# Performance work log

Hardware: AMD Instinct MI355X
Metric: run time of the kernel (lower is better)

## Reference

```python
import jax, jax.numpy as jnp
import numpy as np

B, T, D = 4, 2048, 1024


def ste_sign(x):
    # forward: sign(x); backward: identity (straight-through)
    return jax.lax.stop_gradient(jnp.sign(x) - x) + x


def setup_inputs() -> dict:
    key = jax.random.key(0)
    kx, kq, kk, kv = jax.random.split(key, 4)
    return {
        "x": jax.random.normal(kx, (B, T, D), dtype=jnp.float32),
        "bv_q": jax.random.normal(kq, (D,), dtype=jnp.float32) * 0.02,
        "bv_k": jax.random.normal(kk, (D,), dtype=jnp.float32) * 0.02,
        "bv_v": jax.random.normal(kv, (D,), dtype=jnp.float32) * 0.02,
    }


def reference(x, bv_q, bv_k, bv_v):
    d = x.shape[-1]
    scale = d ** (-0.5)
    bq = ste_sign(bv_q)
    bk = ste_sign(bv_k)
    bv = ste_sign(bv_v)
    Q = ste_sign(x * bq)          # [B,T,D], values in {-1,0,1}
    K = ste_sign(x * bk)
    V = x * bv                    # [B,T,D]
    scores = jnp.einsum('btd,bsd->bts', Q, K) * scale  # [B,T,T]
    t = x.shape[1]
    causal = jnp.tril(jnp.ones((t, t), dtype=bool))    # [T,T]
    scores = jnp.where(causal, scores, -jnp.inf)
    attn = jax.nn.sigmoid(scores * 4.0)
    attn = jnp.where(causal, attn, 0.0)
    return jnp.einsum('bts,bsd->btd', attn, V)
```

## Files before the change

### kernel.cpp

```cpp
#include <hip/hip_runtime.h>
#include <hip/hip_bf16.h>
#include <stdint.h>
#include <math.h>

#define B_SZ 4
#define T_SZ 2048
#define D_SZ 1024

constexpr int NTH = 512;

typedef short bf16x8 __attribute__((ext_vector_type(8)));
typedef float f32x4 __attribute__((ext_vector_type(4)));
typedef int i32x4 __attribute__((ext_vector_type(4)));
typedef unsigned short ushort8 __attribute__((ext_vector_type(8)));

__device__ __forceinline__ uint32_t sbf(uint32_t xu, uint32_t su) {
  return 0x3F80u | (((xu ^ su) >> 16) & 0x8000u);
}

__device__ __forceinline__ ushort f2bf(float f) {
  uint32_t u = __float_as_uint(f);
  return (ushort)((u + 0x7FFFu + ((u >> 16) & 1u)) >> 16);
}

__device__ __forceinline__ void glds16(const void* g, void* l) {
  __builtin_amdgcn_global_load_lds(
      (const __attribute__((address_space(1))) void*)g,
      (__attribute__((address_space(3))) void*)l, 16, 0, 0);
}

__global__ __launch_bounds__(256) void prep_kernel(
    const float* __restrict__ x, const float* __restrict__ bvq,
    const float* __restrict__ bvk, const float* __restrict__ bvv,
    char* __restrict__ Qb, char* __restrict__ Kb, ushort* __restrict__ Vt) {
  __shared__ ushort vt[64][72];
  const int bid = blockIdx.x;
  const int dt = bid & 15;
  const int tt = (bid >> 4) & 31;
  const int b = bid >> 9;
  const int t0 = tt * 64, d0 = dt * 64;
  const int tid = threadIdx.x;

#pragma unroll
  for (int p = 0; p < 4; ++p) {
    const int row = p * 16 + (tid >> 4);
    const int c4 = tid & 15;
    const size_t idx = ((size_t)(b * T_SZ + t0 + row)) * D_SZ + d0 + c4 * 4;
    float4 v = *(const float4*)(x + idx);
    float4 q = *(const float4*)(bvq + d0 + c4 * 4);
    float4 k = *(const float4*)(bvk + d0 + c4 * 4);
    float4 s = *(const float4*)(bvv + d0 + c4 * 4);
    uint32_t xu[4] = {__float_as_uint(v.x), __float_as_uint(v.y),
                      __float_as_uint(v.z), __float_as_uint(v.w)};
    uint32_t qu[4] = {__float_as_uint(q.x), __float_as_uint(q.y),
                      __float_as_uint(q.z), __float_as_uint(q.w)};
    uint32_t ku[4] = {__float_as_uint(k.x), __float_as_uint(k.y),
                      __float_as_uint(k.z), __float_as_uint(k.w)};
    uint32_t su[4] = {__float_as_uint(s.x), __float_as_uint(s.y),
                      __float_as_uint(s.z), __float_as_uint(s.w)};
    uint32_t qw = 0, kw = 0;
#pragma unroll
    for (int j = 0; j < 4; ++j) {
      uint32_t qb = ((xu[j] ^ qu[j]) & 0x80000000u) ? 0xFFu : 0x01u;
      uint32_t kb = ((xu[j] ^ ku[j]) & 0x80000000u) ? 0xFFu : 0x01u;
      qw |= qb << (8 * j);
      kw |= kb << (8 * j);
      vt[row][c4 * 4 + j] = f2bf(__uint_as_float(xu[j] ^ (su[j] & 0x80000000u)));
    }
    *(uint32_t*)(Qb + idx) = qw;
    *(uint32_t*)(Kb + idx) = kw;
  }
  __syncthreads();
#pragma unroll
  for (int p = 0; p < 2; ++p) {
    const int dr = p * 32 + (tid >> 3);
    const int tc = tid & 7;
    ushort8 o;
#pragma unroll
    for (int j = 0; j < 8; ++j) o[j] = vt[tc * 8 + j][dr];
    *(ushort8*)(Vt + ((size_t)(b * D_SZ + d0 + dr)) * T_SZ + t0 + tc * 8) = o;
  }
}

__global__ __launch_bounds__(NTH) void score_kernel(
    const char* __restrict__ Qb, const char* __restrict__ Kb,
    ushort* __restrict__ P) {
  __shared__ __align__(16) unsigned char Qs[2][128 * 128];
  __shared__ __align__(16) unsigned char Ks[2][128 * 128];

  const int bid = blockIdx.x;
  const int xcd = bid & 7;
  const int b = xcd >> 1;
  const int j = ((bid >> 3) << 1) + (xcd & 1);
  int qt = (int)((sqrtf(8.f * (float)j + 1.f) - 1.f) * 0.5f);
  while ((qt + 1) * (qt + 2) / 2 <= j) ++qt;
  while (qt * (qt + 1) / 2 > j) --qt;
  const int st = j - qt * (qt + 1) / 2;

  const int tid = threadIdx.x;
  const int lane = tid & 63, w = tid >> 6;
  const int wr = w >> 1, wc = w & 1;
  const int l15 = lane & 15, l4 = lane >> 4;

  const size_t qrow0 = ((size_t)(b * T_SZ + qt * 128)) * D_SZ;
  const size_t krow0 = ((size_t)(b * T_SZ + st * 128)) * D_SZ;

  i32x4 sacc[2][4];
#pragma unroll
  for (int mf = 0; mf < 2; ++mf)
#pragma unroll
    for (int nf = 0; nf < 4; ++nf) sacc[mf][nf] = (i32x4){0, 0, 0, 0};

  auto STAGE = [&](int buf, int ks) {
#pragma unroll
    for (int i = 0; i < 4; ++i) {
      const int isK = i >> 1;
      const int fi = tid + (i & 1) * 512;
      const int row = fi >> 3, c = fi & 7;
      const int cs = c ^ (row & 7);
      const char* src = (isK ? Kb + krow0 : Qb + qrow0) +
                        (size_t)row * D_SZ + ks * 128 + cs * 16;
      unsigned char* dst = (isK ? Ks[buf] : Qs[buf]) + fi * 16;
      glds16(src, dst);
    }
  };

  STAGE(0, 0);
  for (int ks = 0; ks < 8; ++ks) {
    asm volatile("s_waitcnt vmcnt(0)" ::: "memory");
    __builtin_amdgcn_s_barrier();
    if (ks + 1 < 8) STAGE((ks + 1) & 1, ks + 1);
    const int buf = ks & 1;
#pragma unroll
    for (int kc = 0; kc < 2; ++kc) {
      i32x4 af[2], bfr[4];
#pragma unroll
      for (int mf = 0; mf < 2; ++mf) {
        const int row = wr * 32 + mf * 16 + l15;
        const int ch = (kc * 4 + l4) ^ (row & 7);
        af[mf] = *(const i32x4*)(Qs[buf] + row * 128 + ch * 16);
      }
#pragma unroll
      for (int nf = 0; nf < 4; ++nf) {
        const int row = wc * 64 + nf * 16 + l15;
        const int ch = (kc * 4 + l4) ^ (row & 7);
        bfr[nf] = *(const i32x4*)(Ks[buf] + row * 128 + ch * 16);
      }
#pragma unroll
      for (int mf = 0; mf < 2; ++mf)
#pragma unroll
        for (int nf = 0; nf < 4; ++nf)
          sacc[mf][nf] = __builtin_amdgcn_mfma_i32_16x16x64_i8(
              af[mf], bfr[nf], sacc[mf][nf], 0, 0, 0);
    }
    asm volatile("s_waitcnt lgkmcnt(0)" ::: "memory");
  }

#pragma unroll
  for (int mf = 0; mf < 2; ++mf)
#pragma unroll
    for (int nf = 0; nf < 4; ++nf)
#pragma unroll
      for (int r = 0; r < 4; ++r) {
        const int qg = qt * 128 + wr * 32 + mf * 16 + l4 * 4 + r;
        const int sg = st * 128 + wc * 64 + nf * 16 + l15;
        float p = 1.f / (1.f + __expf(-0.125f * (float)sacc[mf][nf][r]));
        if (sg > qg) p = 0.f;
        P[((size_t)(b * T_SZ + qg)) * T_SZ + sg] = f2bf(p);
      }
}

__global__ __launch_bounds__(NTH, 4) void pv_kernel(
    const ushort* __restrict__ P, const ushort* __restrict__ Vt,
    float* __restrict__ out) {
  __shared__ __align__(16) unsigned char Pl[2][64 * 128];
  __shared__ __align__(16) unsigned char Vl[2][256 * 128];
  const int bid = blockIdx.x;
  const int xcd = bid & 7;
  const int t_ = bid >> 3;
  const int g = xcd + 8 * (t_ & 1);
  const int b = g >> 2;
  const int ds = g & 3;
  const int qt = 31 - (t_ >> 1);

  const int tid = threadIdx.x;
  const int lane = tid & 63, w = tid >> 6;
  const int wr = w >> 2, dg = w & 3;
  const int l15 = lane & 15, l4 = lane >> 4;

  const char* Pb = (const char*)P;
  const char* Vb = (const char*)Vt;
  const size_t vrow0 = ((size_t)(b * D_SZ + ds * 256)) * (T_SZ * 2);
  const size_t prow0 = ((size_t)(b * T_SZ + qt * 64)) * (T_SZ * 2);
  const int nst = qt + 1;

  auto STAGE = [&](int buf, int stt) {
    {
      const int row = tid >> 3, c = tid & 7;
      const int cs = c ^ (row & 7);
      glds16(Pb + prow0 + (size_t)row * (T_SZ * 2) + stt * 128 + cs * 16,
             Pl[buf] + tid * 16);
    }
#pragma unroll
    for (int i = 0; i < 4; ++i) {
      const int f = tid + i * 512;
      const int row = f >> 3, c = f & 7;
      const int cs = c ^ (row & 7);
      glds16(Vb + vrow0 + (size_t)row * (T_SZ * 2) + stt * 128 + cs * 16,
             Vl[buf] + f * 16);
    }
  };

  f32x4 acc[2][4];
#pragma unroll
  for (int mf = 0; mf < 2; ++mf)
#pragma unroll
    for (int nf = 0; nf < 4; ++nf) acc[mf][nf] = (f32x4){0.f, 0.f, 0.f, 0.f};

  STAGE(0, 0);

  for (int t = 0; t < nst; ++t) {
    asm volatile("s_waitcnt vmcnt(0)" ::: "memory");
    __builtin_amdgcn_s_barrier();
    if (t + 1 < nst) STAGE((t + 1) & 1, t + 1);
    const int buf = t & 1;
#pragma unroll
    for (int kk = 0; kk < 2; ++kk) {
      bf16x8 pa[2], vb[4];
#pragma unroll
      for (int mf = 0; mf < 2; ++mf) {
        const int row = wr * 32 + mf * 16 + l15;
        const int ch = (kk * 4 + l4) ^ (row & 7);
        pa[mf] = *(const bf16x8*)(Pl[buf] + row * 128 + ch * 16);
      }
#pragma unroll
      for (int nf = 0; nf < 4; ++nf) {
        const int row = dg * 64 + nf * 16 + l15;
        const int ch = (kk * 4 + l4) ^ (row & 7);
        vb[nf] = *(const bf16x8*)(Vl[buf] + row * 128 + ch * 16);
      }
#pragma unroll
      for (int mf = 0; mf < 2; ++mf)
#pragma unroll
        for (int nf = 0; nf < 4; ++nf)
          acc[mf][nf] = __builtin_amdgcn_mfma_f32_16x16x32_bf16(
              pa[mf], vb[nf], acc[mf][nf], 0, 0, 0);
    }
    asm volatile("s_waitcnt lgkmcnt(0)" ::: "memory");
  }

  float* ob = out + ((size_t)(b * T_SZ + qt * 64 + wr * 32)) * D_SZ +
              ds * 256 + dg * 64;
#pragma unroll
  for (int mf = 0; mf < 2; ++mf)
#pragma unroll
    for (int nf = 0; nf < 4; ++nf)
#pragma unroll
      for (int r = 0; r < 4; ++r)
        ob[(size_t)(mf * 16 + l4 * 4 + r) * D_SZ + nf * 16 + l15] =
            acc[mf][nf][r];
}

__global__ __launch_bounds__(NTH, 4) void attn_main(
    const char* __restrict__ Qb, const char* __restrict__ Kb,
    const ushort* __restrict__ Vt, float* __restrict__ out) {
  __shared__ __align__(16) unsigned char Qs[32][1040];
  __shared__ __align__(16) ushort Ps[32][72];
  const int tid = threadIdx.x;
  const int lane = tid & 63;
  const int w = tid >> 6;
  const int rg = w >> 2, cg = w & 3;
  const int l15 = lane & 15, l4 = lane >> 4;
  const int bid = blockIdx.x;
  const int half = bid & 1;
  const int ti = (bid >> 1) & 63;
  const int b = bid >> 7;
  const int t0 = ti * 32;
  {
    const int row = tid >> 4;
    const int c = (tid & 15) * 64;
    const uint4* src = (const uint4*)(Qb + ((size_t)(b * T_SZ + t0 + row)) * D_SZ + c);
    uint4 a0 = src[0], a1 = src[1], a2 = src[2], a3 = src[3];
    *(uint4*)&Qs[row][c] = a0;
    *(uint4*)&Qs[row][c + 16] = a1;
    *(uint4*)&Qs[row][c + 32] = a2;
    *(uint4*)&Qs[row][c + 48] = a3;
  }
  __syncthreads();
  const int nt = (t0 + 32 + 63) / 64;
  const int s_beg = half ? (nt + 1) / 2 : 0;
  const int s_end = half ? nt : (nt + 1) / 2;
  f32x4 acc[16];
#pragma unroll
  for (int f = 0; f < 16; ++f) acc[f] = (f32x4){0.f, 0.f, 0.f, 0.f};
  const unsigned char* qrow = &Qs[rg * 16 + l15][l4 * 16];
  for (int st = s_beg; st < s_end; ++st) {
    const int s0 = st * 64;
    i32x4 sacc = (i32x4){0, 0, 0, 0};
    const char* kbase = Kb + ((size_t)(b * T_SZ + s0 + cg * 16 + l15)) * D_SZ + l4 * 16;
#pragma unroll
    for (int kc = 0; kc < 16; ++kc) {
      i32x4 a = *(const i32x4*)(qrow + kc * 64);
      i32x4 kf = *(const i32x4*)(kbase + kc * 64);
      sacc = __builtin_amdgcn_mfma_i32_16x16x64_i8(a, kf, sacc, 0, 0, 0);
    }
    __syncthreads();
    {
      const int scol = cg * 16 + l15;
      const int sg = s0 + scol;
#pragma unroll
      for (int r = 0; r < 4; ++r) {
        const int m = rg * 16 + l4 * 4 + r;
        float p = 0.f;
        if (sg <= t0 + m) p = 1.f / (1.f + __expf(-0.125f * (float)sacc[r]));
        Ps[m][scol] = f2bf(p);
      }
    }
    __syncthreads();
    const ushort* vtb = Vt + ((size_t)(b * D_SZ + cg * 256)) * T_SZ + s0;
#pragma unroll
    for (int kk = 0; kk < 2; ++kk) {
      bf16x8 pa = *(const bf16x8*)&Ps[rg * 16 + l15][kk * 32 + l4 * 8];
      const ushort* vks = vtb + kk * 32 + l4 * 8;
#pragma unroll
      for (int f = 0; f < 16; ++f) {
        bf16x8 vb = *(const bf16x8*)(vks + (size_t)(f * 16 + l15) * T_SZ);
        acc[f] = __builtin_amdgcn_mfma_f32_16x16x32_bf16(pa, vb, acc[f], 0, 0, 0);
      }
    }
  }
  float* orow = out + ((size_t)(b * T_SZ + t0)) * D_SZ;
#pragma unroll
  for (int f = 0; f < 16; ++f) {
    const int n = cg * 256 + f * 16 + l15;
#pragma unroll
    for (int r = 0; r < 4; ++r) {
      const int m = rg * 16 + l4 * 4 + r;
      atomicAdd(orow + (size_t)m * D_SZ + n, acc[f][r]);
    }
  }
}

__global__ __launch_bounds__(NTH) void hdc_attn_fallback(
    const float* __restrict__ x, const float* __restrict__ bvq,
    const float* __restrict__ bvk, const float* __restrict__ bvv,
    float* __restrict__ out) {
  __shared__ ushort Qs[32][1032];
  __shared__ ushort Ks[64][72];
  __shared__ ushort Ps[32][72];
  const int tid = threadIdx.x;
  const int lane = tid & 63;
  const int w = tid >> 6;
  const int rg = w >> 2, cg = w & 3;
  const int l15 = lane & 15, l4 = lane >> 4;
  const int b = blockIdx.x >> 6;
  const int ti = blockIdx.x & 63;
  const int t0 = ti * 32;
  {
    const float4* xr = (const float4*)(x + ((size_t)b * T_SZ + t0) * D_SZ);
    const float4* bq4 = (const float4*)bvq;
#pragma unroll
    for (int i = 0; i < 16; ++i) {
      int flat4 = tid + i * NTH;
      int row = flat4 >> 8, c4 = flat4 & 255;
      float4 v = xr[row * 256 + c4];
      float4 q = bq4[c4];
      uint32_t q0 = sbf(__float_as_uint(v.x), __float_as_uint(q.x));
      uint32_t q1 = sbf(__float_as_uint(v.y), __float_as_uint(q.y));
      uint32_t q2 = sbf(__float_as_uint(v.z), __float_as_uint(q.z));
      uint32_t q3 = sbf(__float_as_uint(v.w), __float_as_uint(q.w));
      *(uint2*)&Qs[row][c4 * 4] = make_uint2(q0 | (q1 << 16), q2 | (q3 << 16));
    }
  }
  uint32_t vsign[16];
#pragma unroll
  for (int f = 0; f < 16; ++f)
    vsign[f] = __float_as_uint(bvv[cg * 256 + f * 16 + l15]) & 0x80000000u;
  f32x4 acc[16];
#pragma unroll
  for (int f = 0; f < 16; ++f) acc[f] = (f32x4){0.f, 0.f, 0.f, 0.f};
  const int nt = (t0 + 32 + 63) / 64;
  for (int st = 0; st < nt; ++st) {
    const int s0 = st * 64;
    f32x4 sacc = (f32x4){0.f, 0.f, 0.f, 0.f};
    for (int dc = 0; dc < D_SZ / 64; ++dc) {
      __syncthreads();
      {
        const int s = tid >> 3;
        const int c8 = (tid & 7) * 8;
        const float* xk = x + ((size_t)b * T_SZ + s0 + s) * D_SZ + dc * 64 + c8;
        const float* bk = bvk + dc * 64 + c8;
        float4 v0 = *(const float4*)xk;
        float4 v1 = *(const float4*)(xk + 4);
        float4 k0 = *(const float4*)bk;
        float4 k1 = *(const float4*)(bk + 4);
        uint32_t w0 = sbf(__float_as_uint(v0.x), __float_as_uint(k0.x)) |
                      (sbf(__float_as_uint(v0.y), __float_as_uint(k0.y)) << 16);
        uint32_t w1 = sbf(__float_as_uint(v0.z), __float_as_uint(k0.z)) |
                      (sbf(__float_as_uint(v0.w), __float_as_uint(k0.w)) << 16);
        uint32_t w2 = sbf(__float_as_uint(v1.x), __float_as_uint(k1.x)) |
                      (sbf(__float_as_uint(v1.y), __float_as_uint(k1.y)) << 16);
        uint32_t w3 = sbf(__float_as_uint(v1.z), __float_as_uint(k1.z)) |
                      (sbf(__float_as_uint(v1.w), __float_as_uint(k1.w)) << 16);
        *(uint4*)&Ks[s][c8] = make_uint4(w0, w1, w2, w3);
      }
      __syncthreads();
#pragma unroll
      for (int h = 0; h < 2; ++h) {
        bf16x8 a = *(const bf16x8*)&Qs[rg * 16 + l15][dc * 64 + h * 32 + l4 * 8];
        bf16x8 kb = *(const bf16x8*)&Ks[cg * 16 + l15][h * 32 + l4 * 8];
        sacc = __builtin_amdgcn_mfma_f32_16x16x32_bf16(a, kb, sacc, 0, 0, 0);
      }
    }
    {
      const int scol = cg * 16 + l15;
      const int sg = s0 + scol;
#pragma unroll
      for (int r = 0; r < 4; ++r) {
        const int m = rg * 16 + l4 * 4 + r;
        float p = 0.f;
        if (sg <= t0 + m) p = 1.f / (1.f + __expf(-0.125f * sacc[r]));
        Ps[m][scol] = (ushort)(__float_as_uint(p) >> 16);
      }
    }
    __syncthreads();
    const float* xv = x + ((size_t)b * T_SZ + s0) * D_SZ;
#pragma unroll
    for (int kk = 0; kk < 2; ++kk) {
      bf16x8 pa = *(const bf16x8*)&Ps[rg * 16 + l15][kk * 32 + l4 * 8];
      const float* xvs = xv + (size_t)(kk * 32 + l4 * 8) * D_SZ;
#pragma unroll
      for (int f = 0; f < 16; ++f) {
        const int n = cg * 256 + f * 16 + l15;
        const float* xn = xvs + n;
        bf16x8 vb;
#pragma unroll
        for (int i = 0; i < 8; ++i) {
          uint32_t u = __float_as_uint(xn[(size_t)i * D_SZ]) ^ vsign[f];
          vb[i] = (short)(u >> 16);
        }
        acc[f] = __builtin_amdgcn_mfma_f32_16x16x32_bf16(pa, vb, acc[f], 0, 0, 0);
      }
    }
  }
  float* orow = out + ((size_t)b * T_SZ + t0) * D_SZ;
#pragma unroll
  for (int f = 0; f < 16; ++f) {
    const int n = cg * 256 + f * 16 + l15;
#pragma unroll
    for (int r = 0; r < 4; ++r) {
      const int m = rg * 16 + l4 * 4 + r;
      orow[(size_t)m * D_SZ + n] = acc[f][r];
    }
  }
}

extern "C" void kernel_launch(void* const* d_in, const int* in_sizes, int n_in,
                              void* d_out, int out_size, void* d_ws, size_t ws_size,
                              hipStream_t stream) {
  const float* x = (const float*)d_in[0];
  const float* bvq = (const float*)d_in[1];
  const float* bvk = (const float*)d_in[2];
  const float* bvv = (const float*)d_in[3];
  float* out = (float*)d_out;

  const size_t QB_SZ = (size_t)B_SZ * T_SZ * D_SZ;
  const size_t VT_SZ = QB_SZ * 2;
  const size_t P_SZ = (size_t)B_SZ * T_SZ * T_SZ * 2;
  const size_t NEED_MID = QB_SZ * 2 + VT_SZ;
  const size_t NEED_FULL = NEED_MID + P_SZ;

  if (ws_size >= NEED_MID) {
    char* Qb = (char*)d_ws;
    char* Kb = Qb + QB_SZ;
    ushort* Vt = (ushort*)(Kb + QB_SZ);
    hipLaunchKernelGGL(prep_kernel, dim3(B_SZ * 32 * 16), dim3(256), 0, stream,
                       x, bvq, bvk, bvv, Qb, Kb, Vt);
    if (ws_size >= NEED_FULL) {
      ushort* P = (ushort*)((char*)d_ws + NEED_MID);
      hipLaunchKernelGGL(score_kernel, dim3(544), dim3(NTH), 0, stream,
                         Qb, Kb, P);
      hipLaunchKernelGGL(pv_kernel, dim3(512), dim3(NTH), 0, stream,
                         P, Vt, out);
    } else {
      hipMemsetAsync(out, 0, (size_t)out_size * sizeof(float), stream);
      hipLaunchKernelGGL(attn_main, dim3(B_SZ * 64 * 2), dim3(NTH), 0, stream,
                         Qb, Kb, Vt, out);
    }
  } else {
    hipLaunchKernelGGL(hdc_attn_fallback, dim3(B_SZ * 64), dim3(NTH), 0, stream,
                       x, bvq, bvk, bvv, out);
  }
}
```

Before: 74.33 us.

## Store P and V in MFMA-fragment tiled layout and read directly in pv_kernel

prep_kernel and score_kernel now write V and P in a blocked 16x8 fragment layout that matches the MFMA operand shape. This lets pv_kernel load operands straight from global memory with contiguous 16-byte reads instead of staging through LDS. pv_kernel now uses 256 threads with 128-wide d slices, and each block handles a pair of q-tiles (qt and 31-qt) to balance the causal work. The mid-size workspace path with attn_main is removed. Without LDS staging, operand reuse across waves depends on the caches, and the P writes in score_kernel become more scattered.

```diff
diff --git a/kernel.cpp b/kernel.cpp
--- a/kernel.cpp
+++ b/kernel.cpp
@@ -29,10 +29,11 @@
       (__attribute__((address_space(3))) void*)l, 16, 0, 0);
 }
 
+
 __global__ __launch_bounds__(256) void prep_kernel(
     const float* __restrict__ x, const float* __restrict__ bvq,
     const float* __restrict__ bvk, const float* __restrict__ bvv,
-    char* __restrict__ Qb, char* __restrict__ Kb, ushort* __restrict__ Vt) {
+    char* __restrict__ Qb, char* __restrict__ Kb, ushort* __restrict__ Vt2) {
   __shared__ ushort vt[64][72];
   const int bid = blockIdx.x;
   const int dt = bid & 15;
@@ -78,13 +79,17 @@
     ushort8 o;
 #pragma unroll
     for (int j = 0; j < 8; ++j) o[j] = vt[tc * 8 + j][dr];
-    *(ushort8*)(Vt + ((size_t)(b * D_SZ + d0 + dr)) * T_SZ + t0 + tc * 8) = o;
+    const int dglob = d0 + dr;
+    const int s8 = (t0 >> 3) + tc;
+    *(ushort8*)(Vt2 +
+                (((size_t)(b * 64 + (dglob >> 4))) * 256 + s8) * 128 +
+                (dglob & 15) * 8) = o;
   }
 }
 
 __global__ __launch_bounds__(NTH) void score_kernel(
     const char* __restrict__ Qb, const char* __restrict__ Kb,
-    ushort* __restrict__ P) {
+    ushort* __restrict__ P2) {
   __shared__ __align__(16) unsigned char Qs[2][128 * 128];
   __shared__ __align__(16) unsigned char Ks[2][128 * 128];
 
@@ -166,178 +171,71 @@
         const int sg = st * 128 + wc * 64 + nf * 16 + l15;
         float p = 1.f / (1.f + __expf(-0.125f * (float)sacc[mf][nf][r]));
         if (sg > qg) p = 0.f;
-        P[((size_t)(b * T_SZ + qg)) * T_SZ + sg] = f2bf(p);
-      }
-}
-
-__global__ __launch_bounds__(NTH, 4) void pv_kernel(
-    const ushort* __restrict__ P, const ushort* __restrict__ Vt,
+        P2[(((size_t)(b * 128 + (qg >> 4))) * 256 + (sg >> 3)) * 128 +
+           (qg & 15) * 8 + (sg & 7)] = f2bf(p);
+      }
+}
+
+__global__ __launch_bounds__(256) void pv_kernel(
+    const ushort* __restrict__ P2, const ushort* __restrict__ Vt2,
     float* __restrict__ out) {
-  __shared__ __align__(16) unsigned char Pl[2][64 * 128];
-  __shared__ __align__(16) unsigned char Vl[2][256 * 128];
   const int bid = blockIdx.x;
   const int xcd = bid & 7;
-  const int t_ = bid >> 3;
-  const int g = xcd + 8 * (t_ & 1);
-  const int b = g >> 2;
-  const int ds = g & 3;
-  const int qt = 31 - (t_ >> 1);
+  const int k_ = bid >> 3;
+  const int g = xcd + 8 * (k_ & 3);
+  const int pr = k_ >> 2;
+  const int b = g >> 3;
+  const int ds = g & 7;
 
   const int tid = threadIdx.x;
   const int lane = tid & 63, w = tid >> 6;
-  const int wr = w >> 2, dg = w & 3;
+  const int wr = w >> 1, dg = w & 1;
   const int l15 = lane & 15, l4 = lane >> 4;
 
-  const char* Pb = (const char*)P;
-  const char* Vb = (const char*)Vt;
-  const size_t vrow0 = ((size_t)(b * D_SZ + ds * 256)) * (T_SZ * 2);
-  const size_t prow0 = ((size_t)(b * T_SZ + qt * 64)) * (T_SZ * 2);
-  const int nst = qt + 1;
-
-  auto STAGE = [&](int buf, int stt) {
-    {
-      const int row = tid >> 3, c = tid & 7;
-      const int cs = c ^ (row & 7);
-      glds16(Pb + prow0 + (size_t)row * (T_SZ * 2) + stt * 128 + cs * 16,
-             Pl[buf] + tid * 16);
-    }
-#pragma unroll
-    for (int i = 0; i < 4; ++i) {
-      const int f = tid + i * 512;
-      const int row = f >> 3, c = f & 7;
-      const int cs = c ^ (row & 7);
-      glds16(Vb + vrow0 + (size_t)row * (T_SZ * 2) + stt * 128 + cs * 16,
-             Vl[buf] + f * 16);
-    }
-  };
-
-  f32x4 acc[2][4];
-#pragma unroll
-  for (int mf = 0; mf < 2; ++mf)
-#pragma unroll
-    for (int nf = 0; nf < 4; ++nf) acc[mf][nf] = (f32x4){0.f, 0.f, 0.f, 0.f};
-
-  STAGE(0, 0);
-
-  for (int t = 0; t < nst; ++t) {
-    asm volatile("s_waitcnt vmcnt(0)" ::: "memory");
-    __builtin_amdgcn_s_barrier();
-    if (t + 1 < nst) STAGE((t + 1) & 1, t + 1);
-    const int buf = t & 1;
-#pragma unroll
-    for (int kk = 0; kk < 2; ++kk) {
-      bf16x8 pa[2], vb[4];
-#pragma unroll
-      for (int mf = 0; mf < 2; ++mf) {
-        const int row = wr * 32 + mf * 16 + l15;
-        const int ch = (kk * 4 + l4) ^ (row & 7);
-        pa[mf] = *(const bf16x8*)(Pl[buf] + row * 128 + ch * 16);
-      }
-#pragma unroll
-      for (int nf = 0; nf < 4; ++nf) {
-        const int row = dg * 64 + nf * 16 + l15;
-        const int ch = (kk * 4 + l4) ^ (row & 7);
-        vb[nf] = *(const bf16x8*)(Vl[buf] + row * 128 + ch * 16);
-      }
-#pragma unroll
-      for (int mf = 0; mf < 2; ++mf)
+  for (int half = 0; half < 2; ++half) {
+    const int qt = half ? (31 - pr) : pr;
+
+    f32x4 acc[2][4];
+#pragma unroll
+    for (int mf = 0; mf < 2; ++mf)
+#pragma unroll
+      for (int nf = 0; nf < 4; ++nf) acc[mf][nf] = (f32x4){0.f, 0.f, 0.f, 0.f};
+
+    const size_t q4base = (size_t)b * 128 + qt * 4 + wr * 2;
+    const size_t d4base = (size_t)b * 64 + ds * 8 + dg * 4;
+
+    for (int st = 0; st <= qt; ++st) {
+#pragma unroll
+      for (int kk = 0; kk < 2; ++kk) {
+        const int s8 = st * 8 + kk * 4 + l4;
+        bf16x8 pa[2], vb[4];
+#pragma unroll
+        for (int mf = 0; mf < 2; ++mf)
+          pa[mf] = *(const bf16x8*)(P2 + ((q4base + mf) * 256 + s8) * 128 +
+                                    l15 * 8);
 #pragma unroll
         for (int nf = 0; nf < 4; ++nf)
-          acc[mf][nf] = __builtin_amdgcn_mfma_f32_16x16x32_bf16(
-              pa[mf], vb[nf], acc[mf][nf], 0, 0, 0);
-    }
-    asm volatile("s_waitcnt lgkmcnt(0)" ::: "memory");
-  }
-
-  float* ob = out + ((size_t)(b * T_SZ + qt * 64 + wr * 32)) * D_SZ +
-              ds * 256 + dg * 64;
-#pragma unroll
-  for (int mf = 0; mf < 2; ++mf)
-#pragma unroll
-    for (int nf = 0; nf < 4; ++nf)
-#pragma unroll
-      for (int r = 0; r < 4; ++r)
-        ob[(size_t)(mf * 16 + l4 * 4 + r) * D_SZ + nf * 16 + l15] =
-            acc[mf][nf][r];
-}
-
-__global__ __launch_bounds__(NTH, 4) void attn_main(
-    const char* __restrict__ Qb, const char* __restrict__ Kb,
-    const ushort* __restrict__ Vt, float* __restrict__ out) {
-  __shared__ __align__(16) unsigned char Qs[32][1040];
-  __shared__ __align__(16) ushort Ps[32][72];
-  const int tid = threadIdx.x;
-  const int lane = tid & 63;
-  const int w = tid >> 6;
-  const int rg = w >> 2, cg = w & 3;
-  const int l15 = lane & 15, l4 = lane >> 4;
-  const int bid = blockIdx.x;
-  const int half = bid & 1;
-  const int ti = (bid >> 1) & 63;
-  const int b = bid >> 7;
-  const int t0 = ti * 32;
-  {
-    const int row = tid >> 4;
-    const int c = (tid & 15) * 64;
-    const uint4* src = (const uint4*)(Qb + ((size_t)(b * T_SZ + t0 + row)) * D_SZ + c);
-    uint4 a0 = src[0], a1 = src[1], a2 = src[2], a3 = src[3];
-    *(uint4*)&Qs[row][c] = a0;
-    *(uint4*)&Qs[row][c + 16] = a1;
-    *(uint4*)&Qs[row][c + 32] = a2;
-    *(uint4*)&Qs[row][c + 48] = a3;
-  }
-  __syncthreads();
-  const int nt = (t0 + 32 + 63) / 64;
-  const int s_beg = half ? (nt + 1) / 2 : 0;
-  const int s_end = half ? nt : (nt + 1) / 2;
-  f32x4 acc[16];
-#pragma unroll
-  for (int f = 0; f < 16; ++f) acc[f] = (f32x4){0.f, 0.f, 0.f, 0.f};
-  const unsigned char* qrow = &Qs[rg * 16 + l15][l4 * 16];
-  for (int st = s_beg; st < s_end; ++st) {
-    const int s0 = st * 64;
-    i32x4 sacc = (i32x4){0, 0, 0, 0};
-    const char* kbase = Kb + ((size_t)(b * T_SZ + s0 + cg * 16 + l15)) * D_SZ + l4 * 16;
-#pragma unroll
-    for (int kc = 0; kc < 16; ++kc) {
-      i32x4 a = *(const i32x4*)(qrow + kc * 64);
-      i32x4 kf = *(const i32x4*)(kbase + kc * 64);
-      sacc = __builtin_amdgcn_mfma_i32_16x16x64_i8(a, kf, sacc, 0, 0, 0);
-    }
-    __syncthreads();
-    {
-      const int scol = cg * 16 + l15;
-      const int sg = s0 + scol;
-#pragma unroll
-      for (int r = 0; r < 4; ++r) {
-        const int m = rg * 16 + l4 * 4 + r;
-        float p = 0.f;
-        if (sg <= t0 + m) p = 1.f / (1.f + __expf(-0.125f * (float)sacc[r]));
-        Ps[m][scol] = f2bf(p);
-      }
-    }
-    __syncthreads();
-    const ushort* vtb = Vt + ((size_t)(b * D_SZ + cg * 256)) * T_SZ + s0;
-#pragma unroll
-    for (int kk = 0; kk < 2; ++kk) {
-      bf16x8 pa = *(const bf16x8*)&Ps[rg * 16 + l15][kk * 32 + l4 * 8];
-      const ushort* vks = vtb + kk * 32 + l4 * 8;
-#pragma unroll
-      for (int f = 0; f < 16; ++f) {
-        bf16x8 vb = *(const bf16x8*)(vks + (size_t)(f * 16 + l15) * T_SZ);
-        acc[f] = __builtin_amdgcn_mfma_f32_16x16x32_bf16(pa, vb, acc[f], 0, 0, 0);
-      }
-    }
-  }
-  float* orow = out + ((size_t)(b * T_SZ + t0)) * D_SZ;
-#pragma unroll
-  for (int f = 0; f < 16; ++f) {
-    const int n = cg * 256 + f * 16 + l15;
-#pragma unroll
-    for (int r = 0; r < 4; ++r) {
-      const int m = rg * 16 + l4 * 4 + r;
-      atomicAdd(orow + (size_t)m * D_SZ + n, acc[f][r]);
-    }
+          vb[nf] = *(const bf16x8*)(Vt2 + ((d4base + nf) * 256 + s8) * 128 +
+                                    l15 * 8);
+#pragma unroll
+        for (int mf = 0; mf < 2; ++mf)
+#pragma unroll
+          for (int nf = 0; nf < 4; ++nf)
+            acc[mf][nf] = __builtin_amdgcn_mfma_f32_16x16x32_bf16(
+                pa[mf], vb[nf], acc[mf][nf], 0, 0, 0);
+      }
+    }
+
+    float* ob = out + ((size_t)(b * T_SZ + qt * 64 + wr * 32)) * D_SZ +
+                ds * 128 + dg * 64;
+#pragma unroll
+    for (int mf = 0; mf < 2; ++mf)
+#pragma unroll
+      for (int nf = 0; nf < 4; ++nf)
+#pragma unroll
+        for (int r = 0; r < 4; ++r)
+          ob[(size_t)(mf * 16 + l4 * 4 + r) * D_SZ + nf * 16 + l15] =
+              acc[mf][nf][r];
   }
 }
 
@@ -467,26 +365,19 @@
   const size_t QB_SZ = (size_t)B_SZ * T_SZ * D_SZ;
   const size_t VT_SZ = QB_SZ * 2;
   const size_t P_SZ = (size_t)B_SZ * T_SZ * T_SZ * 2;
-  const size_t NEED_MID = QB_SZ * 2 + VT_SZ;
-  const size_t NEED_FULL = NEED_MID + P_SZ;
-
-  if (ws_size >= NEED_MID) {
+  const size_t NEED_FULL = QB_SZ * 2 + VT_SZ + P_SZ;
+
+  if (ws_size >= NEED_FULL) {
     char* Qb = (char*)d_ws;
     char* Kb = Qb + QB_SZ;
-    ushort* Vt = (ushort*)(Kb + QB_SZ);
+    ushort* Vt2 = (ushort*)(Kb + QB_SZ);
+    ushort* P2 = (ushort*)((char*)Vt2 + VT_SZ);
     hipLaunchKernelGGL(prep_kernel, dim3(B_SZ * 32 * 16), dim3(256), 0, stream,
-                       x, bvq, bvk, bvv, Qb, Kb, Vt);
-    if (ws_size >= NEED_FULL) {
-      ushort* P = (ushort*)((char*)d_ws + NEED_MID);
-      hipLaunchKernelGGL(score_kernel, dim3(544), dim3(NTH), 0, stream,
-                         Qb, Kb, P);
-      hipLaunchKernelGGL(pv_kernel, dim3(512), dim3(NTH), 0, stream,
-                         P, Vt, out);
-    } else {
-      hipMemsetAsync(out, 0, (size_t)out_size * sizeof(float), stream);
-      hipLaunchKernelGGL(attn_main, dim3(B_SZ * 64 * 2), dim3(NTH), 0, stream,
-                         Qb, Kb, Vt, out);
-    }
+                       x, bvq, bvk, bvv, Qb, Kb, Vt2);
+    hipLaunchKernelGGL(score_kernel, dim3(544), dim3(NTH), 0, stream,
+                       Qb, Kb, P2);
+    hipLaunchKernelGGL(pv_kernel, dim3(512), dim3(256), 0, stream,
+                       P2, Vt2, out);
   } else {
     hipLaunchKernelGGL(hdc_attn_fallback, dim3(B_SZ * 64), dim3(NTH), 0, stream,
                        x, bvq, bvk, bvv, out);
```

After: 76.97 us. 1.04x slower.
